# Performance work log

Measured on AMD Instinct MI355X. Metric: run time of the kernel, lower is better.

## Reference

```python
import jax, jax.numpy as jnp
import numpy as np

B, D, H, N, K, C = 1024, 256, 512, 100000, 96, 10


def setup_inputs() -> dict:
    key = jax.random.key(0)
    ks = jax.random.split(key, 16)
    s = 0.02
    return {
        "x": jax.random.normal(ks[0], (B, D), jnp.float32),
        "candidate_x": jax.random.normal(ks[1], (N, D), jnp.float32),
        "candidate_labels": jax.random.randint(ks[2], (N,), 0, C, jnp.int32),
        "W_enc": jax.random.normal(ks[3], (D, H), jnp.float32) * s,
        "b_enc": jnp.zeros((H,), jnp.float32),
        "W_key": jax.random.normal(ks[4], (H, H), jnp.float32) * s,
        "b_key": jnp.zeros((H,), jnp.float32),
        "W_val": jax.random.normal(ks[5], (H, H), jnp.float32) * s,
        "b_val": jnp.zeros((H,), jnp.float32),
        "E_label": jax.random.normal(ks[6], (C, H), jnp.float32) * s,
        "W_t1": jax.random.normal(ks[7], (H, H), jnp.float32) * s,
        "b_t1": jnp.zeros((H,), jnp.float32),
        "W_t2": jax.random.normal(ks[8], (H, H), jnp.float32) * s,
    }


def reference(x, candidate_x, candidate_labels, W_enc, b_enc, W_key, b_key,
              W_val, b_val, E_label, W_t1, b_t1, W_t2):
    # Encode queries and candidates
    x_enc = x @ W_enc + b_enc                       # [B, H]
    cand_enc = candidate_x @ W_enc + b_enc          # [N, H]
    x_key = x_enc @ W_key + b_key                   # [B, H]
    cand_keys = cand_enc @ W_key + b_key            # [N, H]

    # Negative euclidean distance via GEMM expansion (compute-efficient cdist)
    q2 = jnp.sum(x_key * x_key, axis=-1, keepdims=True)        # [B, 1]
    c2 = jnp.sum(cand_keys * cand_keys, axis=-1)               # [N]
    d2 = q2 + c2[None, :] - 2.0 * (x_key @ cand_keys.T)        # [B, N]
    sim = -jnp.sqrt(jnp.maximum(d2, 0.0))                      # [B, N]

    # Top-k retrieval
    top_sims, top_idx = jax.lax.top_k(sim, K)                  # [B, K]

    cand_vals = cand_enc @ W_val + b_val                       # [N, H]
    label_emb = E_label[candidate_labels]                      # [N, H]

    ctx_keys = cand_keys[top_idx]                              # [B, K, H]
    ctx_labels = label_emb[top_idx]                            # [B, K, H]
    _ = cand_vals[top_idx]  # gathered values (unused by the original math)

    # Attention over retrieved context (softmax of top-k similarities)
    attn = jax.nn.softmax(top_sims, axis=1)                    # [B, K]

    # Correction MLP T (dropout is identity in eval mode)
    diff = x_key[:, None, :] - ctx_keys                        # [B, K, H]
    t_out = jax.nn.relu(diff @ W_t1 + b_t1) @ W_t2             # [B, K, H]

    ctx_vec = jnp.sum(attn[..., None] * (ctx_labels + t_out), axis=1)  # [B, H]
    return x_enc + ctx_vec
```

## Files before the change

kernel.cpp:

```cpp
#include <hip/hip_runtime.h>
#include <cfloat>
#include <cmath>

#define B_ 1024
#define D_ 256
#define H_ 512
#define N_ 100000
#define K_ 96
#define C_ 10
#define SAMP 4096
#define CAPC 4096
#define RCAP 15

typedef __attribute__((ext_vector_type(8))) short bf16x8;
typedef __attribute__((ext_vector_type(4))) float f32x4;

__device__ __forceinline__ float bf2f(ushort h) {
    union { unsigned u; float f; } v; v.u = ((unsigned)h) << 16; return v.f;
}
__device__ __forceinline__ ushort f2bf(float f) {
    union { float f; unsigned u; } v; v.f = f;
    unsigned u = v.u;
    unsigned r = (u + 0x7fffu + ((u >> 16) & 1u)) >> 16;
    return (ushort)r;
}
__device__ __forceinline__ unsigned f2key(float f) {
    unsigned u = __float_as_uint(f);
    return (u & 0x80000000u) ? ~u : (u | 0x80000000u);
}
__device__ __forceinline__ float d2_of(float acc, float q2, float c2) {
    return fmaxf(fmaf(-2.f, acc, q2 + c2), 0.f);
}

#define GLDS(g, l)                                                            \
    __builtin_amdgcn_global_load_lds(                                         \
        (const __attribute__((address_space(1))) void*)(g),                   \
        (__attribute__((address_space(3))) void*)(l), 16, 0, 0)

#define FENCE() asm volatile("" ::: "memory")

template <int RELU>
__global__ __launch_bounds__(256) void gemm_nn(const float* __restrict__ A,
                                               const float* __restrict__ Bm,
                                               const float* __restrict__ bias,
                                               float* __restrict__ Cm,
                                               int M, int N, int Kd) {
    __shared__ float sA[16][68];
    __shared__ float sB[16][64];
    const int t  = threadIdx.x;
    const int tx = t & 15, ty = t >> 4;
    const int m0 = blockIdx.y * 64;
    const int n0 = blockIdx.x * 64;
    const int lr = t >> 2;
    const int lk = (t & 3) << 2;
    const int bk = t >> 4;
    const int bn = (t & 15) << 2;

    float acc[4][4] = {};
    for (int k0 = 0; k0 < Kd; k0 += 16) {
        float4 av = make_float4(0.f, 0.f, 0.f, 0.f);
        if (m0 + lr < M)
            av = *(const float4*)(A + (size_t)(m0 + lr) * Kd + k0 + lk);
        sA[lk + 0][lr] = av.x; sA[lk + 1][lr] = av.y;
        sA[lk + 2][lr] = av.z; sA[lk + 3][lr] = av.w;
        float4 bv = *(const float4*)(Bm + (size_t)(k0 + bk) * N + n0 + bn);
        *(float4*)&sB[bk][bn] = bv;
        __syncthreads();
#pragma unroll
        for (int kk = 0; kk < 16; ++kk) {
            float4 a4 = *(const float4*)&sA[kk][ty << 2];
            float4 b4 = *(const float4*)&sB[kk][tx << 2];
            float ar[4] = {a4.x, a4.y, a4.z, a4.w};
            float br[4] = {b4.x, b4.y, b4.z, b4.w};
#pragma unroll
            for (int i = 0; i < 4; ++i)
#pragma unroll
                for (int j = 0; j < 4; ++j)
                    acc[i][j] = fmaf(ar[i], br[j], acc[i][j]);
        }
        __syncthreads();
    }
#pragma unroll
    for (int i = 0; i < 4; ++i) {
        int row = m0 + (ty << 2) + i;
        if (row < M) {
            int col = n0 + (tx << 2);
            float b0 = 0.f, b1 = 0.f, b2 = 0.f, b3 = 0.f;
            if (bias) { b0 = bias[col]; b1 = bias[col + 1]; b2 = bias[col + 2]; b3 = bias[col + 3]; }
            float4 o;
            o.x = acc[i][0] + b0; o.y = acc[i][1] + b1;
            o.z = acc[i][2] + b2; o.w = acc[i][3] + b3;
            if (RELU) {
                o.x = fmaxf(o.x, 0.f); o.y = fmaxf(o.y, 0.f);
                o.z = fmaxf(o.z, 0.f); o.w = fmaxf(o.w, 0.f);
            }
            *(float4*)(Cm + (size_t)row * N + col) = o;
        }
    }
}

template <int MODE, int SWZ>
__global__ __launch_bounds__(256) void gemm_nt(const ushort* __restrict__ A,
                                               const ushort* __restrict__ Bv,
                                               const float* __restrict__ bias,
                                               const float* __restrict__ q2v,
                                               const float* __restrict__ c2v,
                                               const float* __restrict__ thrv,
                                               float* __restrict__ candV,
                                               int* __restrict__ candI,
                                               int* __restrict__ cnt,
                                               void* __restrict__ Cout,
                                               int M, int Nlim, int K,
                                               int ldc, int nvalid, int per) {
    int m0, n0;
    if (SWZ == 0) {
        m0 = blockIdx.y * 128; n0 = blockIdx.x * 128;
    } else if (SWZ == 1) {
        int bid = blockIdx.x;
        int xcd = bid & 7, slot = bid >> 3;
        m0 = (slot & 7) * 128;
        n0 = (xcd * per + (slot >> 3)) * 128;
        if (n0 >= nvalid || m0 >= M) return;
    } else {
        int bid = blockIdx.x;
        int xcd = bid & 7, slot = bid >> 3;
        n0 = (slot & 3) * 128;
        m0 = (xcd * per + (slot >> 2)) * 128;
        if (m0 >= M) return;
    }

    __shared__ __align__(16) char smem[32768];
    const int t = threadIdx.x;
    const int lane = t & 63, w = t >> 6;
    const int wm = w & 1, wn = w >> 1;

    f32x4 acc[4][4];
#pragma unroll
    for (int i = 0; i < 4; ++i)
#pragma unroll
        for (int j = 0; j < 4; ++j)
            acc[i][j] = (f32x4){0.f, 0.f, 0.f, 0.f};

    const int la = lane & 15, lk = lane >> 4;
    const int aoff = (wm * 64 + la) * 64 + lk * 16;
    const int boff = (wn * 64 + la) * 64 + lk * 16;
    const int r_ = t >> 2, cc_ = (t & 3);

    auto stage = [&](int k0, int buf) {
#pragma unroll
        for (int q = 0; q < 2; ++q) {
            int r = r_ + q * 64;
            int ar = m0 + r; ar = (ar < M) ? ar : (M - 1);
            GLDS(A + (size_t)ar * K + k0 + cc_ * 8,
                 (char*)smem + buf * 8192 + (q * 256 + t) * 16);
            int br = n0 + r; br = (br < Nlim) ? br : (Nlim - 1);
            GLDS(Bv + (size_t)br * K + k0 + cc_ * 8,
                 (char*)smem + 16384 + buf * 8192 + (q * 256 + t) * 16);
        }
    };

    stage(0, 0);
    int cur = 0;
    for (int k0 = 0; k0 < K; k0 += 32) {
        if (k0 + 32 < K) {
            stage(k0 + 32, cur ^ 1);
            FENCE();
            asm volatile("s_waitcnt vmcnt(4)" ::: "memory");
        } else {
            FENCE();
            asm volatile("s_waitcnt vmcnt(0)" ::: "memory");
        }
        __builtin_amdgcn_s_barrier(); FENCE();

        bf16x8 af[4], bfr[4];
        const char* pA = (const char*)smem + cur * 8192 + aoff;
        const char* pB = (const char*)smem + 16384 + cur * 8192 + boff;
#pragma unroll
        for (int i = 0; i < 4; ++i)
            af[i] = *(const bf16x8*)(pA + i * 1024);
#pragma unroll
        for (int j = 0; j < 4; ++j)
            bfr[j] = *(const bf16x8*)(pB + j * 1024);
#pragma unroll
        for (int i = 0; i < 4; ++i)
#pragma unroll
            for (int j = 0; j < 4; ++j)
                acc[i][j] = __builtin_amdgcn_mfma_f32_16x16x32_bf16(
                    af[i], bfr[j], acc[i][j], 0, 0, 0);

        FENCE();
        asm volatile("s_waitcnt lgkmcnt(0)" ::: "memory");
        __builtin_amdgcn_s_barrier(); FENCE();
        cur ^= 1;
    }

    const int rl = (lane >> 4) * 4, cl = lane & 15;

    if (MODE == 7) {
#pragma unroll
        for (int i = 0; i < 4; ++i) {
#pragma unroll
            for (int v = 0; v < 4; ++v) {
                int gr = m0 + wm * 64 + i * 16 + rl + v;
                float s = 0.f;
#pragma unroll
                for (int j = 0; j < 4; ++j) {
                    int gc = n0 + wn * 64 + j * 16 + cl;
                    float val = acc[i][j][v] + bias[gc];
                    float vb = bf2f(f2bf(val));
                    s = fmaf(vb, vb, s);
                }
                s += __shfl_xor(s, 1);
                s += __shfl_xor(s, 2);
                s += __shfl_xor(s, 4);
                s += __shfl_xor(s, 8);
                if (cl == 0 && gr < M) atomicAdd(&candV[gr], s);
            }
        }
        return;
    }

    if (MODE == 5) {
        float* stV = (float*)smem;
        int*   stI = (int*)(smem + 7680);
        int*   stC = (int*)(smem + 15360);
        for (int r = t; r < 128; r += 256) stC[r] = 0;
        __syncthreads();
#pragma unroll
        for (int i = 0; i < 4; ++i) {
#pragma unroll
            for (int v = 0; v < 4; ++v) {
                int rloc = wm * 64 + i * 16 + rl + v;
                int gr = m0 + rloc;
                float q2b = q2v[gr];
                float th = thrv[gr];
#pragma unroll
                for (int j = 0; j < 4; ++j) {
                    int gc = n0 + wn * 64 + j * 16 + cl;
                    if (gc < nvalid) {
                        float d2 = d2_of(acc[i][j][v], q2b, c2v[gc]);
                        if (d2 <= th) {
                            int p = atomicAdd(&stC[rloc], 1);
                            if (p < RCAP) {
                                stV[rloc * RCAP + p] = d2;
                                stI[rloc * RCAP + p] = gc;
                            } else {
                                int gp = atomicAdd(&cnt[gr], 1);
                                if (gp < CAPC) {
                                    candV[(size_t)gr * CAPC + gp] = d2;
                                    candI[(size_t)gr * CAPC + gp] = gc;
                                }
                            }
                        }
                    }
                }
            }
        }
        __syncthreads();
        for (int r = t; r < 128; r += 256) {
            int n = stC[r]; if (n > RCAP) n = RCAP;
            if (n > 0) {
                int gr = m0 + r;
                int gb = atomicAdd(&cnt[gr], n);
                for (int q = 0; q < n; ++q) {
                    int pos = gb + q;
                    if (pos < CAPC) {
                        candV[(size_t)gr * CAPC + pos] = stV[r * RCAP + q];
                        candI[(size_t)gr * CAPC + pos] = stI[r * RCAP + q];
                    }
                }
            }
        }
        return;
    }

#pragma unroll
    for (int i = 0; i < 4; ++i) {
#pragma unroll
        for (int j = 0; j < 4; ++j) {
            int gc = n0 + wn * 64 + j * 16 + cl;
#pragma unroll
            for (int v = 0; v < 4; ++v) {
                int gr = m0 + wm * 64 + i * 16 + rl + v;
                if (gr < M && gc < nvalid) {
                    float val = acc[i][j][v];
                    if (MODE == 2) {
                        ((float*)Cout)[(size_t)gr * ldc + gc] = val;
                    } else if (MODE == 4) {
                        ((float*)Cout)[(size_t)gr * ldc + gc] = val + bias[gc];
                    } else {
                        if (MODE == 3) val += bias[gc];
                        ((ushort*)Cout)[(size_t)gr * ldc + gc] = f2bf(val);
                    }
                }
            }
        }
    }
}

__global__ __launch_bounds__(256) void thr_select(const float* __restrict__ S,
                                                  int ld,
                                                  const float* __restrict__ q2v,
                                                  const float* __restrict__ c2v,
                                                  float* __restrict__ thrArr) {
    __shared__ unsigned keys[SAMP];
    __shared__ int hist[256];
    __shared__ int sel[2];
    const int b = blockIdx.x, t = threadIdx.x;
    const float q2b = q2v[b];
    for (int i = t; i < SAMP; i += 256)
        keys[i] = ~f2key(d2_of(S[(size_t)b * ld + i], q2b, c2v[i]));
    __syncthreads();
    unsigned prefix = 0, mask = 0;
    int rank = K_;
    for (int shift = 24; shift >= 0; shift -= 8) {
        hist[t & 255] = 0;
        __syncthreads();
        for (int i = t; i < SAMP; i += 256) {
            unsigned k = keys[i];
            if ((k & mask) == prefix) atomicAdd(&hist[(k >> shift) & 255], 1);
        }
        __syncthreads();
        if (t == 0) {
            int r = rank, d = 255;
            for (; d > 0; --d) { int c = hist[d]; if (r - c <= 0) break; r -= c; }
            sel[0] = d; sel[1] = (r < 1) ? 1 : r;
        }
        __syncthreads();
        prefix |= ((unsigned)sel[0]) << shift;
        rank = sel[1];
        mask |= (0xFFu << shift);
        __syncthreads();
    }
    if (t == 0) {
        unsigned key = ~prefix;
        thrArr[b] = __uint_as_float(key & 0x7FFFFFFFu);
    }
}

__global__ __launch_bounds__(256) void final_select(const float* __restrict__ candV,
                                                    const int* __restrict__ candI,
                                                    const int* __restrict__ cnt,
                                                    float* __restrict__ topV,
                                                    int* __restrict__ topI) {
    __shared__ unsigned keys[CAPC];
    __shared__ int hist[256];
    __shared__ int sel[2];
    __shared__ int poscnt, eqcnt;
    const int b = blockIdx.x, t = threadIdx.x;
    int n = cnt[b]; if (n > CAPC) n = CAPC;
    for (int i = t; i < n; i += 256)
        keys[i] = ~f2key(candV[(size_t)b * CAPC + i]);
    __syncthreads();
    unsigned prefix = 0, mask = 0;
    int rank = K_;
    for (int shift = 24; shift >= 0; shift -= 8) {
        hist[t & 255] = 0;
        __syncthreads();
        for (int i = t; i < n; i += 256) {
            unsigned k = keys[i];
            if ((k & mask) == prefix) atomicAdd(&hist[(k >> shift) & 255], 1);
        }
        __syncthreads();
        if (t == 0) {
            int r = rank, d = 255;
            for (; d > 0; --d) { int c = hist[d]; if (r - c <= 0) break; r -= c; }
            sel[0] = d; sel[1] = (r < 1) ? 1 : r;
        }
        __syncthreads();
        prefix |= ((unsigned)sel[0]) << shift;
        rank = sel[1];
        mask |= (0xFFu << shift);
        __syncthreads();
    }
    unsigned kth = prefix;
    if (t == 0) { poscnt = 0; eqcnt = 0; }
    __syncthreads();
    for (int i = t; i < n; i += 256) {
        if (keys[i] > kth) {
            int p = atomicAdd(&poscnt, 1);
            topV[b * K_ + p] = candV[(size_t)b * CAPC + i];
            topI[b * K_ + p] = candI[(size_t)b * CAPC + i];
        }
    }
    __syncthreads();
    int base = poscnt;
    for (int i = t; i < n; i += 256) {
        if (keys[i] == kth) {
            int p = atomicAdd(&eqcnt, 1);
            if (base + p < K_) {
                topV[b * K_ + base + p] = candV[(size_t)b * CAPC + i];
                topI[b * K_ + base + p] = candI[(size_t)b * CAPC + i];
            }
        }
    }
}

__global__ void init_cnt(int* cnt) {
    int i = blockIdx.x * 256 + threadIdx.x;
    if (i < B_) cnt[i] = 0;
}

__global__ void init_f32(float* p, int n) {
    int i = blockIdx.x * 256 + threadIdx.x;
    int stride = gridDim.x * 256;
    for (; i < n; i += stride) p[i] = 0.f;
}

__global__ void conv_f2b(const float* __restrict__ in, ushort* __restrict__ out, int n) {
    int i = (blockIdx.x * 256 + threadIdx.x) * 4;
    int stride = gridDim.x * 256 * 4;
    for (; i < n; i += stride) {
        float4 v = *(const float4*)(in + i);
        ushort4 o;
        o.x = f2bf(v.x); o.y = f2bf(v.y); o.z = f2bf(v.z); o.w = f2bf(v.w);
        *(ushort4*)(out + i) = o;
    }
}

__global__ __launch_bounds__(256) void transpose_f2b(const float* __restrict__ in,
                                                     ushort* __restrict__ out,
                                                     int R, int Cn) {
    __shared__ float tile[32][33];
    int bx = blockIdx.x * 32, by = blockIdx.y * 32;
    int tx = threadIdx.x & 31, ty = threadIdx.x >> 5;
    int x = bx + tx;
#pragma unroll
    for (int dy = 0; dy < 32; dy += 8) {
        int y = by + ty + dy;
        if (x < Cn && y < R) tile[ty + dy][tx] = in[(size_t)y * Cn + x];
    }
    __syncthreads();
    int ox = by + tx;
#pragma unroll
    for (int dy = 0; dy < 32; dy += 8) {
        int oy = bx + ty + dy;
        if (ox < R && oy < Cn) out[(size_t)oy * R + ox] = f2bf(tile[tx][ty + dy]);
    }
}

__global__ __launch_bounds__(64) void q2x_k(const ushort* __restrict__ Xb,
                                            const float* __restrict__ Xf,
                                            const float* __restrict__ bc,
                                            float* __restrict__ outv) {
    const int r = blockIdx.x, t = threadIdx.x;
    const ushort* p  = Xb + (size_t)r * H_ + t * 8;
    const float*  xf = Xf + (size_t)r * H_ + t * 8;
    float nrm = 0.f, dot = 0.f;
#pragma unroll
    for (int j = 0; j < 8; ++j) {
        float v = bf2f(p[j]);
        nrm = fmaf(v, v, nrm);
        dot = fmaf(xf[j], bc[t * 8 + j], dot);
    }
    for (int off = 32; off > 0; off >>= 1) {
        nrm += __shfl_down(nrm, off);
        dot += __shfl_down(dot, off);
    }
    if (t == 0) outv[r] = nrm - 2.f * dot;
}

__global__ void bcomb_k(const float* __restrict__ b_enc,
                        const float* __restrict__ W_key,
                        const float* __restrict__ b_key,
                        float* __restrict__ b_comb) {
    int h = blockIdx.x * 256 + threadIdx.x;
    if (h >= H_) return;
    float acc = b_key[h];
    for (int m = 0; m < H_; ++m)
        acc = fmaf(b_enc[m], W_key[(size_t)m * H_ + h], acc);
    b_comb[h] = acc;
}

__global__ void bq_k(const float* __restrict__ bc,
                     const float* __restrict__ W1,
                     float* __restrict__ bq) {
    int h = blockIdx.x * 256 + threadIdx.x;
    if (h >= H_) return;
    float acc = 0.f;
    for (int m = 0; m < H_; ++m)
        acc = fmaf(bc[m], W1[(size_t)m * H_ + h], acc);
    bq[h] = acc;
}

__global__ __launch_bounds__(128) void softmax_k(const float* __restrict__ topVal,
                                                 float* __restrict__ attn) {
    __shared__ float red[128];
    const int b = blockIdx.x, t = threadIdx.x;
    float v = (t < K_) ? -sqrtf(topVal[b * K_ + t]) : -FLT_MAX;
    red[t] = v; __syncthreads();
    for (int s = 64; s > 0; s >>= 1) {
        if (t < s) red[t] = fmaxf(red[t], red[t + s]);
        __syncthreads();
    }
    float m = red[0]; __syncthreads();
    float e = (t < K_) ? expf(v - m) : 0.f;
    red[t] = e; __syncthreads();
    for (int s = 64; s > 0; s >>= 1) {
        if (t < s) red[t] += red[t + s];
        __syncthreads();
    }
    float ssum = red[0];
    if (t < K_) attn[b * K_ + t] = e / ssum;
}

__global__ __launch_bounds__(256) void wsum_q(const float* __restrict__ attn,
                                              const int* __restrict__ topI,
                                              const float* __restrict__ P,
                                              const ushort* __restrict__ Q,
                                              ushort* __restrict__ hw) {
    __shared__ float aw[K_];
    __shared__ int ai[K_];
    const int b = blockIdx.x, t = threadIdx.x;
    if (t < K_) { aw[t] = attn[b * K_ + t]; ai[t] = topI[b * K_ + t]; }
    __syncthreads();
    const float p0 = P[(size_t)b * H_ + 2 * t];
    const float p1 = P[(size_t)b * H_ + 2 * t + 1];
    float a0 = 0.f, a1 = 0.f;
    for (int k = 0; k < K_; ++k) {
        float w = aw[k];
        ushort2 q = *(const ushort2*)(Q + (size_t)ai[k] * H_ + 2 * t);
        a0 = fmaf(w, fmaxf(p0 - bf2f(q.x), 0.f), a0);
        a1 = fmaf(w, fmaxf(p1 - bf2f(q.y), 0.f), a1);
    }
    ushort2 o; o.x = f2bf(a0); o.y = f2bf(a1);
    *(ushort2*)(hw + (size_t)b * H_ + 2 * t) = o;
}

__global__ __launch_bounds__(256) void final_out(const float* __restrict__ attn,
                                                 const int* __restrict__ topI,
                                                 const int* __restrict__ labels,
                                                 const float* __restrict__ E,
                                                 const float* __restrict__ tsum,
                                                 const float* __restrict__ xe,
                                                 float* __restrict__ out) {
    const int b = blockIdx.x, t = threadIdx.x;
    float a0 = 0.f, a1 = 0.f;
    for (int k = 0; k < K_; ++k) {
        float w = attn[b * K_ + k];
        int idx = topI[b * K_ + k];
        int lab = labels[idx];
        const float* el = E + (size_t)lab * H_;
        a0 = fmaf(w, el[t], a0);
        a1 = fmaf(w, el[t + 256], a1);
    }
    out[(size_t)b * H_ + t] =
        xe[(size_t)b * H_ + t] + a0 + tsum[(size_t)b * H_ + t];
    out[(size_t)b * H_ + t + 256] =
        xe[(size_t)b * H_ + t + 256] + a1 + tsum[(size_t)b * H_ + t + 256];
}

extern "C" void kernel_launch(void* const* d_in, const int* in_sizes, int n_in,
                              void* d_out, int out_size, void* d_ws, size_t ws_size,
                              hipStream_t stream) {
    const float* x      = (const float*)d_in[0];
    const float* cx     = (const float*)d_in[1];
    const int*   labels = (const int*)d_in[2];
    const float* W_enc  = (const float*)d_in[3];
    const float* b_enc  = (const float*)d_in[4];
    const float* W_key  = (const float*)d_in[5];
    const float* b_key  = (const float*)d_in[6];
    const float* E_label = (const float*)d_in[9];
    const float* W_t1   = (const float*)d_in[10];
    const float* b_t1   = (const float*)d_in[11];
    const float* W_t2   = (const float*)d_in[12];
    float* out = (float*)d_out;

    char* base = (char*)d_ws;
    size_t off = 0;
    auto take = [&](size_t n) -> char* {
        char* p = base + off;
        off = (off + n + 255) & ~(size_t)255;
        return p;
    };
    float*  Wc    = (float*)take((size_t)D_ * H_ * 4);
    float*  bc    = (float*)take((size_t)H_ * 4);
    ushort* WcT   = (ushort*)take((size_t)H_ * D_ * 2);
    ushort* Wcb   = (ushort*)take((size_t)D_ * H_ * 2);
    float*  Wq    = (float*)take((size_t)D_ * H_ * 4);
    ushort* WqT   = (ushort*)take((size_t)H_ * D_ * 2);
    float*  bq    = (float*)take((size_t)H_ * 4);
    ushort* Wt1T  = (ushort*)take((size_t)H_ * H_ * 2);
    ushort* Wt2T  = (ushort*)take((size_t)H_ * H_ * 2);
    float*  xe    = (float*)take((size_t)B_ * H_ * 4);
    float*  xk    = (float*)take((size_t)B_ * H_ * 4);
    ushort* xkb   = (ushort*)take((size_t)B_ * H_ * 2);
    ushort* xprojb= (ushort*)take((size_t)B_ * D_ * 2);
    float*  q2x   = (float*)take((size_t)B_ * 4);
    float*  c2    = (float*)take((size_t)N_ * 4);
    float*  topV  = (float*)take((size_t)B_ * K_ * 4);
    int*    topI  = (int*)take((size_t)B_ * K_ * 4);
    float*  thr   = (float*)take((size_t)B_ * 4);
    float*  attn  = (float*)take((size_t)B_ * K_ * 4);
    int*    cnt   = (int*)take((size_t)B_ * 4);
    float*  candV = (float*)take((size_t)B_ * CAPC * 4);
    int*    candI = (int*)take((size_t)B_ * CAPC * 4);
    ushort* hwAll = (ushort*)take((size_t)B_ * H_ * 2);
    float*  tsum  = (float*)take((size_t)B_ * H_ * 4);
    float*  Pbuf  = (float*)take((size_t)B_ * H_ * 4);
    ushort* Qb    = (ushort*)take((size_t)N_ * H_ * 2);
    char*   big   = base + off;

    ushort* cxb = (ushort*)big;
    float* simSmall = (float*)candV;

    {
        dim3 g(H_ / 64, D_ / 64);
        gemm_nn<0><<<g, 256, 0, stream>>>(W_enc, W_key, nullptr, Wc, D_, H_, H_);
        bcomb_k<<<(H_ + 255) / 256, 256, 0, stream>>>(b_enc, W_key, b_key, bc);
        gemm_nn<0><<<g, 256, 0, stream>>>(Wc, W_t1, nullptr, Wq, D_, H_, H_);
        bq_k<<<(H_ + 255) / 256, 256, 0, stream>>>(bc, W_t1, bq);
        dim3 gt1((H_ + 31) / 32, (D_ + 31) / 32);
        transpose_f2b<<<gt1, 256, 0, stream>>>(Wc, WcT, D_, H_);
        transpose_f2b<<<gt1, 256, 0, stream>>>(Wq, WqT, D_, H_);
        conv_f2b<<<128, 256, 0, stream>>>(Wc, Wcb, D_ * H_);
        dim3 gt2((H_ + 31) / 32, (H_ + 31) / 32);
        transpose_f2b<<<gt2, 256, 0, stream>>>(W_t1, Wt1T, H_, H_);
        transpose_f2b<<<gt2, 256, 0, stream>>>(W_t2, Wt2T, H_, H_);
    }
    {
        dim3 gx(H_ / 64, B_ / 64);
        gemm_nn<0><<<gx, 256, 0, stream>>>(x, W_enc, b_enc, xe, B_, H_, D_);
        gemm_nn<0><<<gx, 256, 0, stream>>>(x, Wc, bc, xk, B_, H_, D_);
        conv_f2b<<<1024, 256, 0, stream>>>(xk, xkb, B_ * H_);
        conv_f2b<<<2048, 256, 0, stream>>>(cx, cxb, N_ * D_);
        dim3 gp(D_ / 128, B_ / 128);
        gemm_nt<0, 0><<<gp, 256, 0, stream>>>(
            xkb, Wcb, nullptr, nullptr, nullptr, nullptr, nullptr, nullptr,
            nullptr, xprojb, B_, D_, H_, D_, D_, 0);
        q2x_k<<<B_, 64, 0, stream>>>(xkb, xk, bc, q2x);
        dim3 gq(H_ / 128, B_ / 128);
        gemm_nt<4, 0><<<gq, 256, 0, stream>>>(
            xkb, Wt1T, b_t1, nullptr, nullptr, nullptr, nullptr, nullptr,
            nullptr, Pbuf, B_, H_, H_, H_, H_, 0);
    }
    init_f32<<<128, 256, 0, stream>>>(c2, N_);
    {
        int mt = (N_ + 127) / 128;
        int mper = (mt + 7) / 8;
        gemm_nt<7, 2><<<8 * mper * 4, 256, 0, stream>>>(
            cxb, WcT, bc, nullptr, nullptr, nullptr, c2, nullptr, nullptr,
            nullptr, N_, H_, D_, H_, H_, mper);
    }

    {
        int nper = (SAMP / 128 + 7) / 8;
        gemm_nt<2, 1><<<64 * nper, 256, 0, stream>>>(
            xprojb, cxb, nullptr, nullptr, nullptr, nullptr, nullptr, nullptr,
            nullptr, simSmall, B_, N_, D_, SAMP, SAMP, nper);
        thr_select<<<B_, 256, 0, stream>>>(simSmall, SAMP, q2x, c2, thr);
    }
    init_cnt<<<(B_ + 255) / 256, 256, 0, stream>>>(cnt);
    {
        int NT = (N_ + 127) / 128;
        int nper = (NT + 7) / 8;
        gemm_nt<5, 1><<<64 * nper, 256, 0, stream>>>(
            xprojb, cxb, nullptr, q2x, c2, thr, candV, candI, cnt,
            nullptr, B_, N_, D_, 0, N_, nper);
    }
    {
        int mt = (N_ + 127) / 128;
        int mper = (mt + 7) / 8;
        gemm_nt<3, 2><<<8 * mper * 4, 256, 0, stream>>>(
            cxb, WqT, bq, nullptr, nullptr, nullptr, nullptr, nullptr,
            nullptr, Qb, N_, H_, D_, H_, H_, mper);
    }
    final_select<<<B_, 256, 0, stream>>>(candV, candI, cnt, topV, topI);
    softmax_k<<<B_, 128, 0, stream>>>(topV, attn);

    wsum_q<<<B_, 256, 0, stream>>>(attn, topI, Pbuf, Qb, hwAll);
    {
        dim3 g(H_ / 128, B_ / 128);
        gemm_nt<2, 0><<<g, 256, 0, stream>>>(
            hwAll, Wt2T, nullptr, nullptr, nullptr, nullptr, nullptr, nullptr,
            nullptr, tsum, B_, H_, H_, H_, H_, 0);
    }
    final_out<<<B_, 256, 0, stream>>>(attn, topI, labels, E_label, tsum, xe, out);
}
```

Baseline: 835.8 us.

## Widen big GEMM tiles to 128x256 and fuse query encode GEMMs

Adds a gemm_nt2 kernel with 128x256 output tiles (8 MFMA column fragments per wave, larger LDS double buffer) for the three N-sized GEMMs: candidate norm, threshold filter and Q projection. Each A tile is reused across twice as many columns and half as many blocks are launched. The filter's per-row LDS staging capacity is raised from 15 to 20 entries. Separately, the x@W_enc and x@Wc GEMMs are merged into one GEMM over a packed weight matrix, with strided views consumed downstream. The larger accumulator array raises register pressure and may lower occupancy.

```diff
diff --git a/kernel.cpp b/kernel.cpp
--- a/kernel.cpp
+++ b/kernel.cpp
@@ -11,6 +11,7 @@
 #define SAMP 4096
 #define CAPC 4096
 #define RCAP 15
+#define RCAP2 20
 
 typedef __attribute__((ext_vector_type(8))) short bf16x8;
 typedef __attribute__((ext_vector_type(4))) float f32x4;
@@ -103,30 +104,18 @@
 __global__ __launch_bounds__(256) void gemm_nt(const ushort* __restrict__ A,
                                                const ushort* __restrict__ Bv,
                                                const float* __restrict__ bias,
-                                               const float* __restrict__ q2v,
-                                               const float* __restrict__ c2v,
-                                               const float* __restrict__ thrv,
-                                               float* __restrict__ candV,
-                                               int* __restrict__ candI,
-                                               int* __restrict__ cnt,
                                                void* __restrict__ Cout,
                                                int M, int Nlim, int K,
                                                int ldc, int nvalid, int per) {
     int m0, n0;
     if (SWZ == 0) {
         m0 = blockIdx.y * 128; n0 = blockIdx.x * 128;
-    } else if (SWZ == 1) {
+    } else {
         int bid = blockIdx.x;
         int xcd = bid & 7, slot = bid >> 3;
         m0 = (slot & 7) * 128;
         n0 = (xcd * per + (slot >> 3)) * 128;
         if (n0 >= nvalid || m0 >= M) return;
-    } else {
-        int bid = blockIdx.x;
-        int xcd = bid & 7, slot = bid >> 3;
-        n0 = (slot & 3) * 128;
-        m0 = (xcd * per + (slot >> 2)) * 128;
-        if (m0 >= M) return;
     }
 
     __shared__ __align__(16) char smem[32768];
@@ -196,6 +185,128 @@
 
     const int rl = (lane >> 4) * 4, cl = lane & 15;
 
+#pragma unroll
+    for (int i = 0; i < 4; ++i) {
+#pragma unroll
+        for (int j = 0; j < 4; ++j) {
+            int gc = n0 + wn * 64 + j * 16 + cl;
+#pragma unroll
+            for (int v = 0; v < 4; ++v) {
+                int gr = m0 + wm * 64 + i * 16 + rl + v;
+                if (gr < M && gc < nvalid) {
+                    float val = acc[i][j][v];
+                    if (MODE == 2) {
+                        ((float*)Cout)[(size_t)gr * ldc + gc] = val;
+                    } else if (MODE == 4) {
+                        ((float*)Cout)[(size_t)gr * ldc + gc] = val + bias[gc];
+                    } else {
+                        ((ushort*)Cout)[(size_t)gr * ldc + gc] = f2bf(val);
+                    }
+                }
+            }
+        }
+    }
+}
+
+template <int MODE, int SWZ>
+__global__ __launch_bounds__(256) void gemm_nt2(const ushort* __restrict__ A,
+                                                const ushort* __restrict__ Bv,
+                                                const float* __restrict__ bias,
+                                                const float* __restrict__ q2v,
+                                                const float* __restrict__ c2v,
+                                                const float* __restrict__ thrv,
+                                                float* __restrict__ candV,
+                                                int* __restrict__ candI,
+                                                int* __restrict__ cnt,
+                                                void* __restrict__ Cout,
+                                                int M, int Nlim, int K,
+                                                int ldc, int nvalid, int per) {
+    int m0, n0;
+    {
+        int bid = blockIdx.x;
+        int xcd = bid & 7, slot = bid >> 3;
+        if (SWZ == 1) {
+            m0 = (slot & 7) * 128;
+            n0 = (xcd * per + (slot >> 3)) * 256;
+            if (n0 >= nvalid) return;
+        } else {
+            n0 = (slot & 1) * 256;
+            m0 = (xcd * per + (slot >> 1)) * 128;
+            if (m0 >= M) return;
+        }
+    }
+
+    __shared__ __align__(16) char smem[49152];
+    const int t = threadIdx.x;
+    const int lane = t & 63, w = t >> 6;
+    const int wm = w & 1, wn = w >> 1;
+
+    f32x4 acc[4][8];
+#pragma unroll
+    for (int i = 0; i < 4; ++i)
+#pragma unroll
+        for (int j = 0; j < 8; ++j)
+            acc[i][j] = (f32x4){0.f, 0.f, 0.f, 0.f};
+
+    const int la = lane & 15, lk = lane >> 4;
+    const int aoff = (wm * 64 + la) * 64 + lk * 16;
+    const int boff = (wn * 128 + la) * 64 + lk * 16;
+    const int r_ = t >> 2, cc_ = (t & 3);
+
+    auto stage = [&](int k0, int buf) {
+#pragma unroll
+        for (int q = 0; q < 2; ++q) {
+            int r = r_ + q * 64;
+            int ar = m0 + r; ar = (ar < M) ? ar : (M - 1);
+            GLDS(A + (size_t)ar * K + k0 + cc_ * 8,
+                 (char*)smem + buf * 8192 + (q * 256 + t) * 16);
+        }
+#pragma unroll
+        for (int q = 0; q < 4; ++q) {
+            int r = r_ + q * 64;
+            int br = n0 + r; br = (br < Nlim) ? br : (Nlim - 1);
+            GLDS(Bv + (size_t)br * K + k0 + cc_ * 8,
+                 (char*)smem + 16384 + buf * 16384 + (q * 256 + t) * 16);
+        }
+    };
+
+    stage(0, 0);
+    int cur = 0;
+    for (int k0 = 0; k0 < K; k0 += 32) {
+        if (k0 + 32 < K) {
+            stage(k0 + 32, cur ^ 1);
+            FENCE();
+            asm volatile("s_waitcnt vmcnt(6)" ::: "memory");
+        } else {
+            FENCE();
+            asm volatile("s_waitcnt vmcnt(0)" ::: "memory");
+        }
+        __builtin_amdgcn_s_barrier(); FENCE();
+
+        bf16x8 af[4], bfr[8];
+        const char* pA = (const char*)smem + cur * 8192 + aoff;
+        const char* pB = (const char*)smem + 16384 + cur * 16384 + boff;
+#pragma unroll
+        for (int i = 0; i < 4; ++i)
+            af[i] = *(const bf16x8*)(pA + i * 1024);
+#pragma unroll
+        for (int j = 0; j < 8; ++j)
+            bfr[j] = *(const bf16x8*)(pB + j * 1024);
+#pragma unroll
+        for (int i = 0; i < 4; ++i)
+#pragma unroll
+            for (int j = 0; j < 8; ++j)
+                acc[i][j] = __builtin_amdgcn_mfma_f32_16x16x32_bf16(
+                    af[i], bfr[j], acc[i][j], 0, 0, 0);
+
+        FENCE();
+        asm volatile("s_waitcnt lgkmcnt(0)" ::: "memory");
+        __builtin_amdgcn_s_barrier(); FENCE();
+        cur ^= 1;
+    }
+
+    const int rl = lk * 4, cl = la;
+
     if (MODE == 7) {
 #pragma unroll
         for (int i = 0; i < 4; ++i) {
@@ -204,8 +315,8 @@
                 int gr = m0 + wm * 64 + i * 16 + rl + v;
                 float s = 0.f;
 #pragma unroll
-                for (int j = 0; j < 4; ++j) {
-                    int gc = n0 + wn * 64 + j * 16 + cl;
+                for (int j = 0; j < 8; ++j) {
+                    int gc = n0 + wn * 128 + j * 16 + cl;
                     float val = acc[i][j][v] + bias[gc];
                     float vb = bf2f(f2bf(val));
                     s = fmaf(vb, vb, s);
@@ -222,8 +333,8 @@
 
     if (MODE == 5) {
         float* stV = (float*)smem;
-        int*   stI = (int*)(smem + 7680);
-        int*   stC = (int*)(smem + 15360);
+        int*   stI = (int*)(smem + 128 * RCAP2 * 4);
+        int*   stC = (int*)(smem + 128 * RCAP2 * 8);
         for (int r = t; r < 128; r += 256) stC[r] = 0;
         __syncthreads();
 #pragma unroll
@@ -235,15 +346,15 @@
                 float q2b = q2v[gr];
                 float th = thrv[gr];
 #pragma unroll
-                for (int j = 0; j < 4; ++j) {
-                    int gc = n0 + wn * 64 + j * 16 + cl;
+                for (int j = 0; j < 8; ++j) {
+                    int gc = n0 + wn * 128 + j * 16 + cl;
                     if (gc < nvalid) {
                         float d2 = d2_of(acc[i][j][v], q2b, c2v[gc]);
                         if (d2 <= th) {
                             int p = atomicAdd(&stC[rloc], 1);
-                            if (p < RCAP) {
-                                stV[rloc * RCAP + p] = d2;
-                                stI[rloc * RCAP + p] = gc;
+                            if (p < RCAP2) {
+                                stV[rloc * RCAP2 + p] = d2;
+                                stI[rloc * RCAP2 + p] = gc;
                             } else {
                                 int gp = atomicAdd(&cnt[gr], 1);
                                 if (gp < CAPC) {
@@ -258,15 +369,15 @@
         }
         __syncthreads();
         for (int r = t; r < 128; r += 256) {
-            int n = stC[r]; if (n > RCAP) n = RCAP;
+            int n = stC[r]; if (n > RCAP2) n = RCAP2;
             if (n > 0) {
                 int gr = m0 + r;
                 int gb = atomicAdd(&cnt[gr], n);
                 for (int q = 0; q < n; ++q) {
                     int pos = gb + q;
                     if (pos < CAPC) {
-                        candV[(size_t)gr * CAPC + pos] = stV[r * RCAP + q];
-                        candI[(size_t)gr * CAPC + pos] = stI[r * RCAP + q];
+                        candV[(size_t)gr * CAPC + pos] = stV[r * RCAP2 + q];
+                        candI[(size_t)gr * CAPC + pos] = stI[r * RCAP2 + q];
                     }
                 }
             }
@@ -277,21 +388,14 @@
 #pragma unroll
     for (int i = 0; i < 4; ++i) {
 #pragma unroll
-        for (int j = 0; j < 4; ++j) {
-            int gc = n0 + wn * 64 + j * 16 + cl;
+        for (int j = 0; j < 8; ++j) {
+            int gc = n0 + wn * 128 + j * 16 + cl;
 #pragma unroll
             for (int v = 0; v < 4; ++v) {
                 int gr = m0 + wm * 64 + i * 16 + rl + v;
                 if (gr < M && gc < nvalid) {
-                    float val = acc[i][j][v];
-                    if (MODE == 2) {
-                        ((float*)Cout)[(size_t)gr * ldc + gc] = val;
-                    } else if (MODE == 4) {
-                        ((float*)Cout)[(size_t)gr * ldc + gc] = val + bias[gc];
-                    } else {
-                        if (MODE == 3) val += bias[gc];
-                        ((ushort*)Cout)[(size_t)gr * ldc + gc] = f2bf(val);
-                    }
+                    float val = acc[i][j][v] + bias[gc];
+                    ((ushort*)Cout)[(size_t)gr * ldc + gc] = f2bf(val);
                 }
             }
         }
@@ -418,6 +522,20 @@
     }
 }
 
+__global__ void conv_f2b_s(const float* __restrict__ in, ushort* __restrict__ out,
+                           int ldin) {
+    int i = (blockIdx.x * 256 + threadIdx.x) * 4;
+    int stride = gridDim.x * 256 * 4;
+    int total = B_ * H_;
+    for (; i < total; i += stride) {
+        int r = i >> 9, c = i & 511;
+        float4 v = *(const float4*)(in + (size_t)r * ldin + c);
+        ushort4 o;
+        o.x = f2bf(v.x); o.y = f2bf(v.y); o.z = f2bf(v.z); o.w = f2bf(v.w);
+        *(ushort4*)(out + i) = o;
+    }
+}
+
 __global__ __launch_bounds__(256) void transpose_f2b(const float* __restrict__ in,
                                                      ushort* __restrict__ out,
                                                      int R, int Cn) {
@@ -439,13 +557,28 @@
     }
 }
 
+__global__ void pack_wxx(const float* __restrict__ W_enc,
+                         const float* __restrict__ Wc,
+                         const float* __restrict__ b_enc,
+                         const float* __restrict__ bc,
+                         float* __restrict__ Wxx, float* __restrict__ bxx) {
+    int i = blockIdx.x * 256 + threadIdx.x;
+    if (i < D_ * H_) {
+        int k = i >> 9, h = i & 511;
+        Wxx[(size_t)k * 1024 + h] = W_enc[i];
+        Wxx[(size_t)k * 1024 + 512 + h] = Wc[i];
+    }
+    if (i < H_) { bxx[i] = b_enc[i]; bxx[512 + i] = bc[i]; }
+}
+
 __global__ __launch_bounds__(64) void q2x_k(const ushort* __restrict__ Xb,
                                             const float* __restrict__ Xf,
+                                            int ldx,
                                             const float* __restrict__ bc,
                                             float* __restrict__ outv) {
     const int r = blockIdx.x, t = threadIdx.x;
     const ushort* p  = Xb + (size_t)r * H_ + t * 8;
-    const float*  xf = Xf + (size_t)r * H_ + t * 8;
+    const float*  xf = Xf + (size_t)r * ldx + t * 8;
     float nrm = 0.f, dot = 0.f;
 #pragma unroll
     for (int j = 0; j < 8; ++j) {
@@ -533,6 +666,7 @@
                                                  const float* __restrict__ E,
                                                  const float* __restrict__ tsum,
                                                  const float* __restrict__ xe,
+                                                 int ldxe,
                                                  float* __restrict__ out) {
     const int b = blockIdx.x, t = threadIdx.x;
     float a0 = 0.f, a1 = 0.f;
@@ -545,9 +679,9 @@
         a1 = fmaf(w, el[t + 256], a1);
     }
     out[(size_t)b * H_ + t] =
-        xe[(size_t)b * H_ + t] + a0 + tsum[(size_t)b * H_ + t];
+        xe[(size_t)b * ldxe + t] + a0 + tsum[(size_t)b * H_ + t];
     out[(size_t)b * H_ + t + 256] =
-        xe[(size_t)b * H_ + t + 256] + a1 + tsum[(size_t)b * H_ + t + 256];
+        xe[(size_t)b * ldxe + t + 256] + a1 + tsum[(size_t)b * H_ + t + 256];
 }
 
 extern "C" void kernel_launch(void* const* d_in, const int* in_sizes, int n_in,
@@ -575,6 +709,8 @@
     };
     float*  Wc    = (float*)take((size_t)D_ * H_ * 4);
     float*  bc    = (float*)take((size_t)H_ * 4);
+    float*  Wxx   = (float*)take((size_t)D_ * 1024 * 4);
+    float*  bxx   = (float*)take((size_t)1024 * 4);
     ushort* WcT   = (ushort*)take((size_t)H_ * D_ * 2);
     ushort* Wcb   = (ushort*)take((size_t)D_ * H_ * 2);
     float*  Wq    = (float*)take((size_t)D_ * H_ * 4);
@@ -582,8 +718,7 @@
     float*  bq    = (float*)take((size_t)H_ * 4);
     ushort* Wt1T  = (ushort*)take((size_t)H_ * H_ * 2);
     ushort* Wt2T  = (ushort*)take((size_t)H_ * H_ * 2);
-    float*  xe    = (float*)take((size_t)B_ * H_ * 4);
-    float*  xk    = (float*)take((size_t)B_ * H_ * 4);
+    float*  xekk  = (float*)take((size_t)B_ * 1024 * 4);
     ushort* xkb   = (ushort*)take((size_t)B_ * H_ * 2);
     ushort* xprojb= (ushort*)take((size_t)B_ * D_ * 2);
     float*  q2x   = (float*)take((size_t)B_ * 4);
@@ -604,12 +739,17 @@
     ushort* cxb = (ushort*)big;
     float* simSmall = (float*)candV;
 
+    const float* xeView = xekk;
+    const float* xkView = xekk + 512;
+
     {
         dim3 g(H_ / 64, D_ / 64);
         gemm_nn<0><<<g, 256, 0, stream>>>(W_enc, W_key, nullptr, Wc, D_, H_, H_);
         bcomb_k<<<(H_ + 255) / 256, 256, 0, stream>>>(b_enc, W_key, b_key, bc);
         gemm_nn<0><<<g, 256, 0, stream>>>(Wc, W_t1, nullptr, Wq, D_, H_, H_);
         bq_k<<<(H_ + 255) / 256, 256, 0, stream>>>(bc, W_t1, bq);
+        pack_wxx<<<(D_ * H_ + 255) / 256, 256, 0, stream>>>(W_enc, Wc, b_enc,
+                                                            bc, Wxx, bxx);
         dim3 gt1((H_ + 31) / 32, (D_ + 31) / 32);
         transpose_f2b<<<gt1, 256, 0, stream>>>(Wc, WcT, D_, H_);
         transpose_f2b<<<gt1, 256, 0, stream>>>(Wq, WqT, D_, H_);
@@ -619,49 +759,44 @@
         transpose_f2b<<<gt2, 256, 0, stream>>>(W_t2, Wt2T, H_, H_);
     }
     {
-        dim3 gx(H_ / 64, B_ / 64);
-        gemm_nn<0><<<gx, 256, 0, stream>>>(x, W_enc, b_enc, xe, B_, H_, D_);
-        gemm_nn<0><<<gx, 256, 0, stream>>>(x, Wc, bc, xk, B_, H_, D_);
-        conv_f2b<<<1024, 256, 0, stream>>>(xk, xkb, B_ * H_);
+        dim3 gx(1024 / 64, B_ / 64);
+        gemm_nn<0><<<gx, 256, 0, stream>>>(x, Wxx, bxx, xekk, B_, 1024, D_);
+        conv_f2b_s<<<1024, 256, 0, stream>>>(xkView, xkb, 1024);
         conv_f2b<<<2048, 256, 0, stream>>>(cx, cxb, N_ * D_);
         dim3 gp(D_ / 128, B_ / 128);
         gemm_nt<0, 0><<<gp, 256, 0, stream>>>(
-            xkb, Wcb, nullptr, nullptr, nullptr, nullptr, nullptr, nullptr,
-            nullptr, xprojb, B_, D_, H_, D_, D_, 0);
-        q2x_k<<<B_, 64, 0, stream>>>(xkb, xk, bc, q2x);
+            xkb, Wcb, nullptr, xprojb, B_, D_, H_, D_, D_, 0);
+        q2x_k<<<B_, 64, 0, stream>>>(xkb, xkView, 1024, bc, q2x);
         dim3 gq(H_ / 128, B_ / 128);
         gemm_nt<4, 0><<<gq, 256, 0, stream>>>(
-            xkb, Wt1T, b_t1, nullptr, nullptr, nullptr, nullptr, nullptr,
-            nullptr, Pbuf, B_, H_, H_, H_, H_, 0);
+            xkb, Wt1T, b_t1, Pbuf, B_, H_, H_, H_, H_, 0);
     }
     init_f32<<<128, 256, 0, stream>>>(c2, N_);
     {
         int mt = (N_ + 127) / 128;
         int mper = (mt + 7) / 8;
-        gemm_nt<7, 2><<<8 * mper * 4, 256, 0, stream>>>(
+        gemm_nt2<7, 2><<<8 * mper * 2, 256, 0, stream>>>(
             cxb, WcT, bc, nullptr, nullptr, nullptr, c2, nullptr, nullptr,
             nullptr, N_, H_, D_, H_, H_, mper);
     }
-
     {
         int nper = (SAMP / 128 + 7) / 8;
         gemm_nt<2, 1><<<64 * nper, 256, 0, stream>>>(
-            xprojb, cxb, nullptr, nullptr, nullptr, nullptr, nullptr, nullptr,
-            nullptr, simSmall, B_, N_, D_, SAMP, SAMP, nper);
+            xprojb, cxb, nullptr, simSmall, B_, N_, D_, SAMP, SAMP, nper);
         thr_select<<<B_, 256, 0, stream>>>(simSmall, SAMP, q2x, c2, thr);
     }
     init_cnt<<<(B_ + 255) / 256, 256, 0, stream>>>(cnt);
     {
-        int NT = (N_ + 127) / 128;
+        int NT = (N_ + 255) / 256;
         int nper = (NT + 7) / 8;
-        gemm_nt<5, 1><<<64 * nper, 256, 0, stream>>>(
+        gemm_nt2<5, 1><<<64 * nper, 256, 0, stream>>>(
             xprojb, cxb, nullptr, q2x, c2, thr, candV, candI, cnt,
             nullptr, B_, N_, D_, 0, N_, nper);
     }
     {
         int mt = (N_ + 127) / 128;
         int mper = (mt + 7) / 8;
-        gemm_nt<3, 2><<<8 * mper * 4, 256, 0, stream>>>(
+        gemm_nt2<3, 2><<<8 * mper * 2, 256, 0, stream>>>(
             cxb, WqT, bq, nullptr, nullptr, nullptr, nullptr, nullptr,
             nullptr, Qb, N_, H_, D_, H_, H_, mper);
     }
@@ -672,8 +807,8 @@
     {
         dim3 g(H_ / 128, B_ / 128);
         gemm_nt<2, 0><<<g, 256, 0, stream>>>(
-            hwAll, Wt2T, nullptr, nullptr, nullptr, nullptr, nullptr, nullptr,
-            nullptr, tsum, B_, H_, H_, H_, H_, 0);
-    }
-    final_out<<<B_, 256, 0, stream>>>(attn, topI, labels, E_label, tsum, xe, out);
-}
+            hwAll, Wt2T, nullptr, tsum, B_, H_, H_, H_, H_, 0);
+    }
+    final_out<<<B_, 256, 0, stream>>>(attn, topI, labels, E_label, tsum,
+                                      xeView, 1024, out);
+}
```

Result: slower. 1.109 ms (+32.7%).
